# Performance work log

Hardware: AMD Instinct MI355X
Metric: run time of the kernel (lower is better)

Reference implementation:

```python
import jax, jax.numpy as jnp
import numpy as np

H = 16      # num_head
DH = 64     # d_head
D = H * DH  # d_model
NEG = -10000.0


def _proj(x, W, b):
    # torch Linear: y = x @ W^T + b
    return jnp.einsum('bld,od->blo', x, W) + b


def _heads(x):
    b, l, _ = x.shape
    return x.reshape(b, l, H, DH)


def _attn_logits(feat_q, mask_q, feat_k, mask_k, Wq, bq, Wk, bk):
    q = _heads(_proj(feat_q, Wq, bq))   # b lq h dh
    k = _heads(_proj(feat_k, Wk, bk))   # b lk h dh
    logits = jnp.einsum('bqhd,bkhd->bhqk', q, k)
    m = mask_q[:, None, :, None] & mask_k[:, None, None, :]  # b 1 lq lk
    return jnp.where(m, logits, NEG)


def setup_inputs() -> dict:
    key = jax.random.key(0)
    ks = jax.random.split(key, 12)
    B, Lv, Lt = 4, 1024, 256
    scale = 1.0 / np.sqrt(D).astype(np.float32)
    inp = {
        'vid_feat': jax.random.normal(ks[0], (B, Lv, D), jnp.float32),
        'vid_mask': jax.random.bernoulli(ks[1], 0.9, (B, Lv)),
        'txt_feat': jax.random.normal(ks[2], (B, Lt, D), jnp.float32),
        'txt_mask': jax.random.bernoulli(ks[3], 0.9, (B, Lt)),
    }
    names = ['v2v', 't2v', 'v2t', 't2t']
    for i, n in enumerate(names):
        inp['W_' + n] = jax.random.normal(ks[4 + i], (3, D, D), jnp.float32) * scale
        inp['b_' + n] = jax.random.normal(ks[8 + i], (3, D), jnp.float32) * 0.01
    return inp


def reference(vid_feat, vid_mask, txt_feat, txt_mask,
              W_v2v, b_v2v, W_t2v, b_t2v, W_v2t, b_v2t, W_t2t, b_t2t):
    B, Lv, _ = vid_feat.shape
    B, Lt, _ = txt_feat.shape
    # sr_ratio == 1: vid_feat_sr == vid_feat, vid_mask_sr == vid_mask
    vid_feat_sr, vid_mask_sr = vid_feat, vid_mask

    # values (proj index 2), concatenated along key length
    v_value = jnp.concatenate([_proj(vid_feat_sr, W_v2v[2], b_v2v[2]),
                               _proj(txt_feat, W_t2v[2], b_t2v[2])], axis=1)
    v_value = _heads(v_value)  # b (Lv+Lt) h dh
    t_value = jnp.concatenate([_proj(vid_feat_sr, W_v2t[2], b_v2t[2]),
                               _proj(txt_feat, W_t2t[2], b_t2t[2])], axis=1)
    t_value = _heads(t_value)

    v2v = _attn_logits(vid_feat, vid_mask, vid_feat_sr, vid_mask_sr,
                       W_v2v[0], b_v2v[0], W_v2v[1], b_v2v[1])
    t2v = _attn_logits(vid_feat, vid_mask, txt_feat, txt_mask,
                       W_t2v[0], b_t2v[0], W_t2v[1], b_t2v[1])
    v2t = _attn_logits(txt_feat, txt_mask, vid_feat_sr, vid_mask_sr,
                       W_v2t[0], b_v2t[0], W_v2t[1], b_v2t[1])
    t2t = _attn_logits(txt_feat, txt_mask, txt_feat, txt_mask,
                       W_t2t[0], b_t2t[0], W_t2t[1], b_t2t[1])

    v_logits = jnp.concatenate([v2v, t2v], axis=-1)  # b h Lv (Lv+Lt)
    t_logits = jnp.concatenate([v2t, t2t], axis=-1)  # b h Lt (Lv+Lt)
    inv_sqrt_dh = jnp.float32(1.0 / np.sqrt(DH))

    # NOTE: original applies softmax, THEN divides by sqrt(d_head) (faithful)
    vid_out = jnp.einsum('bhqk,bkhd->bqhd',
                         jax.nn.softmax(v_logits, axis=-1) * inv_sqrt_dh,
                         v_value).reshape(B, Lv, D)
    txt_out = jnp.einsum('bhqk,bkhd->bqhd',
                         jax.nn.softmax(t_logits, axis=-1) * inv_sqrt_dh,
                         t_value).reshape(B, Lt, D)
    return vid_out, txt_out
```

## Files before the change

kernel.cpp:

```cpp
#include <hip/hip_runtime.h>


typedef __attribute__((ext_vector_type(8))) _Float16  half8;
typedef __attribute__((ext_vector_type(4))) _Float16  half4;
typedef __attribute__((ext_vector_type(4))) float     f32x4;
typedef __attribute__((ext_vector_type(4))) unsigned int uint4v;
typedef __attribute__((ext_vector_type(2))) unsigned int uint2v;

#define MFMA_F16   __builtin_amdgcn_mfma_f32_16x16x32_f16
#define MFMA16_F16 __builtin_amdgcn_mfma_f32_16x16x16f16

static __device__ __forceinline__ unsigned short f_to_f16u(float f) {
  _Float16 h = (_Float16)f;
  return __builtin_bit_cast(unsigned short, h);
}

#define GLOAD_LDS16(g, l)                                            \
  __builtin_amdgcn_global_load_lds(                                  \
      (const __attribute__((address_space(1))) void*)(g),            \
      (__attribute__((address_space(3))) void*)(l), 16, 0, 0)

struct CvtDesc { const float* src; unsigned short* dst; int n8; };
struct CvtArgs { CvtDesc d[14]; };

__global__ __launch_bounds__(256) void cvt_fp16(CvtArgs ca) {
  const CvtDesc dd = ca.d[blockIdx.y];
  const int stride = gridDim.x * blockDim.x;
  for (int i = blockIdx.x * blockDim.x + threadIdx.x; i < dd.n8; i += stride) {
    const f32x4 a = ((const f32x4*)dd.src)[i * 2];
    const f32x4 b = ((const f32x4*)dd.src)[i * 2 + 1];
    half8 h;
    h[0] = (_Float16)a[0]; h[1] = (_Float16)a[1];
    h[2] = (_Float16)a[2]; h[3] = (_Float16)a[3];
    h[4] = (_Float16)b[0]; h[5] = (_Float16)b[1];
    h[6] = (_Float16)b[2]; h[7] = (_Float16)b[3];
    ((half8*)dd.dst)[i] = h;
  }
}

__global__ __launch_bounds__(256) void make_kbias(
    const int* __restrict__ vmask, const int* __restrict__ tmask,
    float* __restrict__ kb) {
  const int b = blockIdx.y;
  const int k = blockIdx.x * 256 + threadIdx.x;
  if (k >= 1280) return;
  const int m = (k < 1024) ? vmask[b * 1024 + k] : tmask[b * 256 + k - 1024];
  kb[b * 1280 + k] = m ? 0.0f : -10000.0f;
}

static __device__ __forceinline__ void copy_out_tile(
    const unsigned short* Cs, unsigned short* dst, int tid,
    int b, int l0, int h0, int Ld, int soff, int mode) {
  for (int i = 0; i < 8; ++i) {
    const int c     = i * 256 + tid;
    const int major = c >> 4;
    const int kc    = c & 15;
    if (mode == 1) {
      const int base = (kc >> 2) * 32 + (kc & 3) * 4;
      const int sw   = major & 7;
      const int o1   = major * 136 + (((base >> 3) ^ sw) << 3) + (base & 7);
      const int b2   = base + 16;
      const int o2   = major * 136 + (((b2 >> 3) ^ sw) << 3) + (b2 & 7);
      const uint2v lo = *(const uint2v*)&Cs[o1];
      const uint2v hi = *(const uint2v*)&Cs[o2];
      uint4v val; val[0] = lo[0]; val[1] = lo[1]; val[2] = hi[0]; val[3] = hi[1];
      const int hh = h0 + (major >> 6);
      const int dh = major & 63;
      const int k  = soff + l0 + (kc >> 2) * 32;
      const size_t el = (size_t)(b * 16 + hh) * 81920 + (size_t)(k >> 5) * 2048 +
                        dh * 32 + (kc & 3) * 8;
      *(uint4v*)(dst + el) = val;
    } else {
      const uint4v val =
          *(const uint4v*)&Cs[major * 136 + ((kc ^ (major & 7)) << 3)];
      if (mode == 0) {
        const size_t el =
            ((size_t)(b * 16 + h0 + (kc >> 3)) * Ld + soff + l0 + major) * 64 +
            (kc & 7) * 8;
        *(uint4v*)(dst + el) = val;
      } else {
        const int k   = soff + l0 + major;
        const int dh0 = (kc & 7) * 8;
        const size_t el = (size_t)(b * 16 + h0 + (kc >> 3)) * 81920 +
                          (size_t)(k >> 4) * 1024 + (dh0 >> 5) * 512 +
                          (k & 15) * 32 + ((dh0 >> 3) & 3) * 8;
        *(uint4v*)(dst + el) = val;
      }
    }
  }
}

struct ProjDescH {
  const unsigned short* X;
  const unsigned short* W;
  const float* Bv;
  unsigned short* dst;
  int M, lxsh, Ld, soff, mode;
};
struct ProjArgsH { ProjDescH d[12]; };

__global__ __launch_bounds__(256) void proj_gemm_h(ProjArgsH pa) {
  const ProjDescH dd = pa.d[blockIdx.z];
  const int m0 = blockIdx.y * 128;
  if (m0 >= dd.M) return;
  const int n0 = blockIdx.x * 128;

  __shared__ __align__(16) unsigned char smem[34816];
  unsigned short* As = (unsigned short*)smem;
  unsigned short* Bs = As + 4096;
  unsigned short* Cs = (unsigned short*)smem;

  const int tid  = threadIdx.x;
  const int lane = tid & 63;
  const int w    = tid >> 6;
  const int wr   = (w >> 1) * 64;
  const int wc   = (w & 1) * 64;
  const int ql   = lane & 15;
  const int qd   = lane >> 4;

  f32x4 acc[4][4];
  for (int i = 0; i < 4; ++i)
    for (int j = 0; j < 4; ++j) acc[i][j] = (f32x4)(0.0f);

  const unsigned short* Xg = dd.X + (size_t)m0 * 1024;
  const unsigned short* Wg = dd.W + (size_t)n0 * 1024;

  for (int k0 = 0; k0 < 1024; k0 += 32) {
    __syncthreads();
    for (int half = 0; half < 2; ++half) {
      const int cb  = w * 128 + half * 64;
      const int c   = cb + lane;
      const int row = c >> 2;
      const int kcg = (c & 3) ^ (row & 3);
      GLOAD_LDS16(Xg + row * 1024 + k0 + kcg * 8, As + cb * 8);
      GLOAD_LDS16(Wg + row * 1024 + k0 + kcg * 8, Bs + cb * 8);
    }
    __syncthreads();

    half8 af[4], bf[4];
    for (int mt = 0; mt < 4; ++mt) {
      const int row = wr + mt * 16 + ql;
      af[mt] = *(const half8*)&As[row * 32 + ((qd ^ (row & 3)) << 3)];
    }
    for (int nt = 0; nt < 4; ++nt) {
      const int row = wc + nt * 16 + ql;
      bf[nt] = *(const half8*)&Bs[row * 32 + ((qd ^ (row & 3)) << 3)];
    }
    for (int mt = 0; mt < 4; ++mt)
      for (int nt = 0; nt < 4; ++nt)
        acc[mt][nt] = MFMA_F16(af[mt], bf[nt], acc[mt][nt], 0, 0, 0);
  }

  float bv[4];
  for (int nt = 0; nt < 4; ++nt)
    bv[nt] = dd.Bv[n0 + wc + nt * 16 + ql];

  __syncthreads();

  for (int mt = 0; mt < 4; ++mt) {
    for (int nt = 0; nt < 4; ++nt) {
      const int nl = wc + nt * 16 + ql;
      for (int r = 0; r < 4; ++r) {
        const int ml = wr + mt * 16 + qd * 4 + r;
        const int row = dd.mode == 1 ? nl : ml;
        const int col = dd.mode == 1 ? ml : nl;
        const float v = acc[mt][nt][r] + bv[nt];
        Cs[row * 136 + (((col >> 3) ^ (row & 7)) << 3) + (col & 7)] = f_to_f16u(v);
      }
    }
  }
  __syncthreads();

  copy_out_tile(Cs, dd.dst, tid, m0 >> dd.lxsh, m0 & ((1 << dd.lxsh) - 1),
                n0 >> 6, dd.Ld, dd.soff, dd.mode);
}

struct ProjDesc {
  const float* X;
  const float* W;
  const float* Bv;
  unsigned short* dst;
  int M, lxsh, Ld, soff, mode;
};
struct ProjArgs { ProjDesc d[12]; };

static __device__ __forceinline__ half8 cvt8sw(const float* base, int row, int g0) {
  const int sw = row & 7;
  const f32x4 a = *(const f32x4*)(base + (row * 8 + (g0 ^ sw)) * 4);
  const f32x4 b = *(const f32x4*)(base + (row * 8 + ((g0 + 1) ^ sw)) * 4);
  half8 h;
  h[0] = (_Float16)a[0]; h[1] = (_Float16)a[1];
  h[2] = (_Float16)a[2]; h[3] = (_Float16)a[3];
  h[4] = (_Float16)b[0]; h[5] = (_Float16)b[1];
  h[6] = (_Float16)b[2]; h[7] = (_Float16)b[3];
  return h;
}

__global__ __launch_bounds__(256) void proj_gemm_f32(ProjArgs pa) {
  const ProjDesc dd = pa.d[blockIdx.z];
  const int m0 = blockIdx.y * 128;
  if (m0 >= dd.M) return;
  const int n0 = blockIdx.x * 128;

  __shared__ __align__(16) unsigned char smem[34816];
  float* As = (float*)smem;
  float* Bs = As + 4096;
  unsigned short* Cs = (unsigned short*)smem;

  const int tid  = threadIdx.x;
  const int lane = tid & 63;
  const int w    = tid >> 6;
  const int wr   = (w >> 1) * 64;
  const int wc   = (w & 1) * 64;
  const int ql   = lane & 15;
  const int qd   = lane >> 4;

  f32x4 acc[4][4];
  for (int i = 0; i < 4; ++i)
    for (int j = 0; j < 4; ++j) acc[i][j] = (f32x4)(0.0f);

  const float* Xg = dd.X + (size_t)m0 * 1024;
  const float* Wg = dd.W + (size_t)n0 * 1024;

  for (int k0 = 0; k0 < 1024; k0 += 32) {
    __syncthreads();
    for (int j = 0; j < 4; ++j) {
      const int cb  = (j * 4 + w) * 64;
      const int c   = cb + lane;
      const int row = c >> 3;
      const int kcg = (c & 7) ^ (row & 7);
      GLOAD_LDS16(Xg + row * 1024 + k0 + kcg * 4, As + cb * 4);
      GLOAD_LDS16(Wg + row * 1024 + k0 + kcg * 4, Bs + cb * 4);
    }
    __syncthreads();

    half8 af[4], bf[4];
    for (int mt = 0; mt < 4; ++mt)
      af[mt] = cvt8sw(As, wr + mt * 16 + ql, qd * 2);
    for (int nt = 0; nt < 4; ++nt)
      bf[nt] = cvt8sw(Bs, wc + nt * 16 + ql, qd * 2);
    for (int mt = 0; mt < 4; ++mt)
      for (int nt = 0; nt < 4; ++nt)
        acc[mt][nt] = MFMA_F16(af[mt], bf[nt], acc[mt][nt], 0, 0, 0);
  }

  float bv[4];
  for (int nt = 0; nt < 4; ++nt)
    bv[nt] = dd.Bv[n0 + wc + nt * 16 + ql];

  __syncthreads();

  for (int mt = 0; mt < 4; ++mt) {
    for (int nt = 0; nt < 4; ++nt) {
      const int nl = wc + nt * 16 + ql;
      for (int r = 0; r < 4; ++r) {
        const int ml = wr + mt * 16 + qd * 4 + r;
        const int row = dd.mode == 1 ? nl : ml;
        const int col = dd.mode == 1 ? ml : nl;
        const float v = acc[mt][nt][r] + bv[nt];
        Cs[row * 136 + (((col >> 3) ^ (row & 7)) << 3) + (col & 7)] = f_to_f16u(v);
      }
    }
  }
  __syncthreads();

  copy_out_tile(Cs, dd.dst, tid, m0 >> dd.lxsh, m0 & ((1 << dd.lxsh) - 1),
                n0 >> 6, dd.Ld, dd.soff, dd.mode);
}

__global__ __launch_bounds__(256) void attn_flash6(
    const unsigned short* __restrict__ Qa_v, const unsigned short* __restrict__ Qb_v,
    const unsigned short* __restrict__ K_v,  const unsigned short* __restrict__ V_vT,
    const unsigned short* __restrict__ Qa_t, const unsigned short* __restrict__ Qb_t,
    const unsigned short* __restrict__ K_t,  const unsigned short* __restrict__ V_tT,
    const int* __restrict__ vmask, const int* __restrict__ tmask,
    const float* __restrict__ kbias,
    float* __restrict__ out_v, float* __restrict__ out_t) {
  __shared__ __align__(16) unsigned short KVs[8192];

  const int bid = blockIdx.x;
  const int sid = (bid & 7) * 160 + (bid >> 3);
  const int bh  = sid / 20;
  const int sub = sid - bh * 20;

  const bool vside = sub < 16;
  const int  Lq    = vside ? 1024 : 256;
  const int  qblk  = vside ? sub : sub - 16;
  const unsigned short* Qa = vside ? Qa_v : Qa_t;
  const unsigned short* Qb = vside ? Qb_v : Qb_t;
  const unsigned short* K  = vside ? K_v  : K_t;
  const unsigned short* VT = vside ? V_vT : V_tT;
  const int* mq  = vside ? vmask : tmask;
  float*     out = vside ? out_v : out_t;

  const int b = bh >> 4;
  const int h = bh & 15;
  const int tid  = threadIdx.x;
  const int w    = tid >> 6;
  const int lane = tid & 63;
  const int ql = lane & 15, qd = lane >> 4;
  const int q0 = qblk * 64 + w * 16;

  const unsigned short* Kb = K  + (size_t)bh * 81920;
  const unsigned short* Vb = VT + (size_t)bh * 81920;
  const float* kbb = kbias + b * 1280;

  const int gsw  = (tid ^ ((tid >> 3) & 3)) * 8;
  const int wlds = w * 512;

#define STAGE6(nb, k0s)                                                     \
  do {                                                                      \
    const unsigned short* Kt_ = Kb + (size_t)((k0s) >> 4) * 1024;           \
    const unsigned short* Vt_ = Vb + (size_t)((k0s) >> 5) * 2048;           \
    unsigned short* Ld_ = KVs + (nb) * 4096 + wlds;                         \
    GLOAD_LDS16(Kt_ + gsw, Ld_);                                            \
    GLOAD_LDS16(Vt_ + gsw, Ld_ + 2048);                                     \
  } while (0)

  STAGE6(0, 0);

  const unsigned short* Qab = Qa + ((size_t)bh * Lq + q0) * 64;
  const unsigned short* Qbb = Qb + ((size_t)bh * Lq + q0) * 64;
  half8 aA[2], aB[2];
  for (int ks = 0; ks < 2; ++ks) {
    aA[ks] = *(const half8*)&Qab[ql * 64 + ks * 32 + qd * 8];
    aB[ks] = *(const half8*)&Qbb[ql * 64 + ks * 32 + qd * 8];
  }
  const int mqs = mq[b * Lq + q0 + ql];

  const int swc = (qd ^ ((ql >> 1) & 3)) * 8;

  float m = -1e30f, l = 0.0f;
  f32x4 o[4];
  for (int nt = 0; nt < 4; ++nt) o[nt] = (f32x4)(0.0f);

  int cur = 0;
  for (int t = 0; t < 40; ++t) {
    __syncthreads();
    if (t < 39) STAGE6(cur ^ 1, (t + 1) * 32);

    const unsigned short* Ls = KVs + cur * 4096;
    const int k0 = t * 32;
    const bool vidp = k0 < 1024;

    half8 vv[4];
    for (int nt = 0; nt < 4; ++nt)
      vv[nt] = *(const half8*)&Ls[2048 + (nt * 16 + ql) * 32 + swc];

    f32x4 sv[2];
    for (int s = 0; s < 2; ++s) {
      f32x4 S = *(const f32x4*)&kbb[k0 + s * 16 + qd * 4];
      const half8 kf0 = *(const half8*)&Ls[s * 1024 + ql * 32 + swc];
      const half8 kf1 = *(const half8*)&Ls[s * 1024 + 512 + ql * 32 + swc];
      if (vidp) { S = MFMA_F16(kf0, aA[0], S, 0, 0, 0); S = MFMA_F16(kf1, aA[1], S, 0, 0, 0); }
      else      { S = MFMA_F16(kf0, aB[0], S, 0, 0, 0); S = MFMA_F16(kf1, aB[1], S, 0, 0, 0); }
      for (int r = 0; r < 4; ++r)
        sv[s][r] = mqs ? S[r] : -10000.0f;
    }

    float bm = fmaxf(fmaxf(fmaxf(sv[0][0], sv[0][1]), fmaxf(sv[0][2], sv[0][3])),
                     fmaxf(fmaxf(sv[1][0], sv[1][1]), fmaxf(sv[1][2], sv[1][3])));
    bm = fmaxf(bm, __shfl_xor(bm, 16, 64));
    bm = fmaxf(bm, __shfl_xor(bm, 32, 64));

    if (__any(bm > m)) {
      const float nm = fmaxf(m, bm);
      const float alpha = __expf(m - nm);
      l *= alpha;
      for (int nt = 0; nt < 4; ++nt)
        for (int r = 0; r < 4; ++r) o[nt][r] *= alpha;
      m = nm;
    }

    half4 pv[2];
    float lsum = 0.0f;
    for (int s = 0; s < 2; ++s)
      for (int r = 0; r < 4; ++r) {
        const float p = __expf(sv[s][r] - m);
        lsum += p;
        pv[s][r] = (_Float16)p;
      }
    l += lsum;

    for (int nt = 0; nt < 4; ++nt) {
      const half4 vlo = __builtin_shufflevector(vv[nt], vv[nt], 0, 1, 2, 3);
      const half4 vhi = __builtin_shufflevector(vv[nt], vv[nt], 4, 5, 6, 7);
      o[nt] = MFMA16_F16(vlo, pv[0], o[nt], 0, 0, 0);
      o[nt] = MFMA16_F16(vhi, pv[1], o[nt], 0, 0, 0);
    }
    cur ^= 1;
  }
#undef STAGE6

  l += __shfl_xor(l, 16, 64);
  l += __shfl_xor(l, 32, 64);
  const float inv = 0.125f / l;

  float* ob = out + ((size_t)(b * Lq + q0 + ql)) * 1024 + h * 64;
  for (int nt = 0; nt < 4; ++nt) {
    f32x4 r;
    for (int j = 0; j < 4; ++j) r[j] = o[nt][j] * inv;
    *(f32x4*)(ob + nt * 16 + qd * 4) = r;
  }
}

extern "C" void kernel_launch(void* const* d_in, const int* in_sizes, int n_in,
                              void* d_out, int out_size, void* d_ws, size_t ws_size,
                              hipStream_t stream) {
  const float* vid   = (const float*)d_in[0];
  const int*   vmask = (const int*)d_in[1];
  const float* txt   = (const float*)d_in[2];
  const int*   tmask = (const int*)d_in[3];
  const float* Wsrc[4] = {(const float*)d_in[4], (const float*)d_in[6],
                          (const float*)d_in[8], (const float*)d_in[10]};
  const float* Bsrc[4] = {(const float*)d_in[5], (const float*)d_in[7],
                          (const float*)d_in[9], (const float*)d_in[11]};

  const int DD = 1024 * 1024, Dm = 1024, MEG = 1048576;

  unsigned short* ws = (unsigned short*)d_ws;
  unsigned short* Qa_v = ws;
  unsigned short* Qb_v = ws + 4194304;
  unsigned short* K_v  = ws + 8388608;
  unsigned short* V_vT = ws + 13631488;
  unsigned short* Qa_t = ws + 18874368;
  unsigned short* Qb_t = ws + 19922944;
  unsigned short* K_t  = ws + 20971520;
  unsigned short* V_tT = ws + 26214400;
  unsigned short* Xv_h = ws + 31457280;
  unsigned short* Xt_h = ws + 35651584;
  unsigned short* Wh   = ws + 36700160;
  float* kbias = (float*)(ws + 31457280);

  const size_t need = (size_t)49283072 * 2;
  const bool use_h = ws_size >= need;

  if (use_h) {
    CvtArgs ca;
    ca.d[0] = CvtDesc{vid, Xv_h, 4194304 / 8};
    ca.d[1] = CvtDesc{txt, Xt_h, 1048576 / 8};
    for (int s = 0; s < 4; ++s)
      for (int j = 0; j < 3; ++j)
        ca.d[2 + s * 3 + j] = CvtDesc{Wsrc[s] + j * DD, Wh + (s * 3 + j) * MEG, DD / 8};
    cvt_fp16<<<dim3(256, 14), dim3(256), 0, stream>>>(ca);

    ProjArgsH pa;
    auto set = [&](int i, const unsigned short* X, int wi, const float* Bv,
                   unsigned short* dst, int M, int lxsh, int Ld, int soff, int mode) {
      pa.d[i] = ProjDescH{X, Wh + wi * MEG, Bv, dst, M, lxsh, Ld, soff, mode};
    };
    set(0,  Xv_h, 0,  Bsrc[0],          Qa_v, 4096, 10, 1024, 0,    0);
    set(1,  Xv_h, 1,  Bsrc[0] + Dm,     K_v,  4096, 10, 1280, 0,    2);
    set(2,  Xv_h, 2,  Bsrc[0] + 2 * Dm, V_vT, 4096, 10, 1280, 0,    1);
    set(3,  Xv_h, 3,  Bsrc[1],          Qb_v, 4096, 10, 1024, 0,    0);
    set(4,  Xt_h, 4,  Bsrc[1] + Dm,     K_v,  1024, 8,  1280, 1024, 2);
    set(5,  Xt_h, 5,  Bsrc[1] + 2 * Dm, V_vT, 1024, 8,  1280, 1024, 1);
    set(6,  Xt_h, 6,  Bsrc[2],          Qa_t, 1024, 8,  256,  0,    0);
    set(7,  Xv_h, 7,  Bsrc[2] + Dm,     K_t,  4096, 10, 1280, 0,    2);
    set(8,  Xv_h, 8,  Bsrc[2] + 2 * Dm, V_tT, 4096, 10, 1280, 0,    1);
    set(9,  Xt_h, 9,  Bsrc[3],          Qb_t, 1024, 8,  256,  0,    0);
    set(10, Xt_h, 10, Bsrc[3] + Dm,     K_t,  1024, 8,  1280, 1024, 2);
    set(11, Xt_h, 11, Bsrc[3] + 2 * Dm, V_tT, 1024, 8,  1280, 1024, 1);

    proj_gemm_h<<<dim3(8, 32, 12), dim3(256), 0, stream>>>(pa);
  } else {
    ProjArgs pa;
    auto set = [&](int i, const float* X, const float* W, const float* Bv,
                   unsigned short* dst, int M, int lxsh, int Ld, int soff, int mode) {
      pa.d[i] = ProjDesc{X, W, Bv, dst, M, lxsh, Ld, soff, mode};
    };
    set(0,  vid, Wsrc[0],          Bsrc[0],          Qa_v, 4096, 10, 1024, 0,    0);
    set(1,  vid, Wsrc[0] + DD,     Bsrc[0] + Dm,     K_v,  4096, 10, 1280, 0,    2);
    set(2,  vid, Wsrc[0] + 2 * DD, Bsrc[0] + 2 * Dm, V_vT, 4096, 10, 1280, 0,    1);
    set(3,  vid, Wsrc[1],          Bsrc[1],          Qb_v, 4096, 10, 1024, 0,    0);
    set(4,  txt, Wsrc[1] + DD,     Bsrc[1] + Dm,     K_v,  1024, 8,  1280, 1024, 2);
    set(5,  txt, Wsrc[1] + 2 * DD, Bsrc[1] + 2 * Dm, V_vT, 1024, 8,  1280, 1024, 1);
    set(6,  txt, Wsrc[2],          Bsrc[2],          Qa_t, 1024, 8,  256,  0,    0);
    set(7,  vid, Wsrc[2] + DD,     Bsrc[2] + Dm,     K_t,  4096, 10, 1280, 0,    2);
    set(8,  vid, Wsrc[2] + 2 * DD, Bsrc[2] + 2 * Dm, V_tT, 4096, 10, 1280, 0,    1);
    set(9,  txt, Wsrc[3],          Bsrc[3],          Qb_t, 1024, 8,  256,  0,    0);
    set(10, txt, Wsrc[3] + DD,     Bsrc[3] + Dm,     K_t,  1024, 8,  1280, 1024, 2);
    set(11, txt, Wsrc[3] + 2 * DD, Bsrc[3] + 2 * Dm, V_tT, 1024, 8,  1280, 1024, 1);

    proj_gemm_f32<<<dim3(8, 32, 12), dim3(256), 0, stream>>>(pa);
  }

  make_kbias<<<dim3(5, 4), dim3(256), 0, stream>>>(vmask, tmask, kbias);

  float* out_v = (float*)d_out;
  float* out_t = out_v + 4 * 1024 * 1024;
  attn_flash6<<<dim3(1280), dim3(256), 0, stream>>>(
      Qa_v, Qb_v, K_v, V_vT, Qa_t, Qb_t, K_t, V_tT,
      vmask, tmask, kbias, out_v, out_t);
}
```

Baseline: 309.2 us.

## Double-buffer LDS staging in fp16 projection GEMM and swap grid axes

Result: slower. 320.9 us (+3.8%).

```diff
diff --git a/kernel.cpp b/kernel.cpp
--- a/kernel.cpp
+++ b/kernel.cpp
@@ -101,13 +101,12 @@
 
 __global__ __launch_bounds__(256) void proj_gemm_h(ProjArgsH pa) {
   const ProjDescH dd = pa.d[blockIdx.z];
-  const int m0 = blockIdx.y * 128;
+  const int m0 = blockIdx.x * 128;
   if (m0 >= dd.M) return;
-  const int n0 = blockIdx.x * 128;
+  const int n0 = blockIdx.y * 128;
 
   __shared__ __align__(16) unsigned char smem[34816];
-  unsigned short* As = (unsigned short*)smem;
-  unsigned short* Bs = As + 4096;
+  unsigned short* AB = (unsigned short*)smem;
   unsigned short* Cs = (unsigned short*)smem;
 
   const int tid  = threadIdx.x;
@@ -125,31 +124,41 @@
   const unsigned short* Xg = dd.X + (size_t)m0 * 1024;
   const unsigned short* Wg = dd.W + (size_t)n0 * 1024;
 
+#define STAGEP(nb, k0s)                                                      \
+  do {                                                                       \
+    unsigned short* Ab_ = AB + (nb) * 8192;                                  \
+    for (int half_ = 0; half_ < 2; ++half_) {                                \
+      const int cb_  = w * 128 + half_ * 64;                                 \
+      const int c_   = cb_ + lane;                                           \
+      const int row_ = c_ >> 2;                                              \
+      const int kcg_ = (c_ & 3) ^ ((c_ >> 3) & 3);                           \
+      GLOAD_LDS16(Xg + row_ * 1024 + (k0s) + kcg_ * 8, Ab_ + cb_ * 8);       \
+      GLOAD_LDS16(Wg + row_ * 1024 + (k0s) + kcg_ * 8, Ab_ + 4096 + cb_ * 8);\
+    }                                                                        \
+  } while (0)
+
+  STAGEP(0, 0);
+
+  const int cpos = (qd ^ ((ql >> 1) & 3)) << 3;
+
+  int cur = 0;
   for (int k0 = 0; k0 < 1024; k0 += 32) {
     __syncthreads();
-    for (int half = 0; half < 2; ++half) {
-      const int cb  = w * 128 + half * 64;
-      const int c   = cb + lane;
-      const int row = c >> 2;
-      const int kcg = (c & 3) ^ (row & 3);
-      GLOAD_LDS16(Xg + row * 1024 + k0 + kcg * 8, As + cb * 8);
-      GLOAD_LDS16(Wg + row * 1024 + k0 + kcg * 8, Bs + cb * 8);
-    }
-    __syncthreads();
-
+    if (k0 + 32 < 1024) STAGEP(cur ^ 1, k0 + 32);
+
+    const unsigned short* As = AB + cur * 8192;
+    const unsigned short* Bs = As + 4096;
     half8 af[4], bf[4];
-    for (int mt = 0; mt < 4; ++mt) {
-      const int row = wr + mt * 16 + ql;
-      af[mt] = *(const half8*)&As[row * 32 + ((qd ^ (row & 3)) << 3)];
-    }
-    for (int nt = 0; nt < 4; ++nt) {
-      const int row = wc + nt * 16 + ql;
-      bf[nt] = *(const half8*)&Bs[row * 32 + ((qd ^ (row & 3)) << 3)];
-    }
+    for (int mt = 0; mt < 4; ++mt)
+      af[mt] = *(const half8*)&As[(wr + mt * 16 + ql) * 32 + cpos];
+    for (int nt = 0; nt < 4; ++nt)
+      bf[nt] = *(const half8*)&Bs[(wc + nt * 16 + ql) * 32 + cpos];
     for (int mt = 0; mt < 4; ++mt)
       for (int nt = 0; nt < 4; ++nt)
         acc[mt][nt] = MFMA_F16(af[mt], bf[nt], acc[mt][nt], 0, 0, 0);
-  }
+    cur ^= 1;
+  }
+#undef STAGEP
 
   float bv[4];
   for (int nt = 0; nt < 4; ++nt)
@@ -198,9 +207,9 @@
 
 __global__ __launch_bounds__(256) void proj_gemm_f32(ProjArgs pa) {
   const ProjDesc dd = pa.d[blockIdx.z];
-  const int m0 = blockIdx.y * 128;
+  const int m0 = blockIdx.x * 128;
   if (m0 >= dd.M) return;
-  const int n0 = blockIdx.x * 128;
+  const int n0 = blockIdx.y * 128;
 
   __shared__ __align__(16) unsigned char smem[34816];
   float* As = (float*)smem;
@@ -462,7 +471,7 @@
     set(10, Xt_h, 10, Bsrc[3] + Dm,     K_t,  1024, 8,  1280, 1024, 2);
     set(11, Xt_h, 11, Bsrc[3] + 2 * Dm, V_tT, 1024, 8,  1280, 1024, 1);
 
-    proj_gemm_h<<<dim3(8, 32, 12), dim3(256), 0, stream>>>(pa);
+    proj_gemm_h<<<dim3(32, 8, 12), dim3(256), 0, stream>>>(pa);
   } else {
     ProjArgs pa;
     auto set = [&](int i, const float* X, const float* W, const float* Bv,
@@ -482,7 +491,7 @@
     set(10, txt, Wsrc[3] + DD,     Bsrc[3] + Dm,     K_t,  1024, 8,  1280, 1024, 2);
     set(11, txt, Wsrc[3] + 2 * DD, Bsrc[3] + 2 * Dm, V_tT, 1024, 8,  1280, 1024, 1);
 
-    proj_gemm_f32<<<dim3(8, 32, 12), dim3(256), 0, stream>>>(pa);
+    proj_gemm_f32<<<dim3(32, 8, 12), dim3(256), 0, stream>>>(pa);
   }
 
   make_kbias<<<dim3(5, 4), dim3(256), 0, stream>>>(vmask, tmask, kbias);
```
